# Kernel tuning notes

Measured on AMD Instinct MI355X. Metric: run time of the kernel, lower is better.

The kernel has to match this reference:

```python
import jax, jax.numpy as jnp
import numpy as np

B, S, D, H, O = 8192, 64, 128, 128, 128  # sets, max set size, input_dim, hidden_dim, out_dim


def setup_inputs() -> dict:
    key = jax.random.key(0)
    ks = jax.random.split(key, 10)
    neigh = jax.random.normal(ks[0], (B, S, D), dtype=jnp.float32)
    lengths = jax.random.randint(ks[1], (B,), 1, S + 1)  # each set has >= 1 neighbor

    def lin_w(k, fan_in, fan_out):
        return jax.random.normal(k, (fan_in, fan_out), dtype=jnp.float32) / np.sqrt(fan_in)

    Wq = lin_w(ks[2], D, H); bq = jax.random.normal(ks[3], (H,), dtype=jnp.float32) * 0.01
    Wk = lin_w(ks[4], D, H); bk = jax.random.normal(ks[5], (H,), dtype=jnp.float32) * 0.01
    Wv = lin_w(ks[6], D, H); bv = jax.random.normal(ks[7], (H,), dtype=jnp.float32) * 0.01
    Wo = lin_w(ks[8], H, O); bo = jax.random.normal(ks[9], (O,), dtype=jnp.float32) * 0.01
    return dict(neigh=neigh, lengths=lengths, Wq=Wq, bq=bq, Wk=Wk, bk=bk,
                Wv=Wv, bv=bv, Wo=Wo, bo=bo)


def reference(neigh, lengths, Wq, bq, Wk, bk, Wv, bv, Wo, bo):
    # neigh: [B, S, D] padded ragged sets; lengths: [B] valid neighbor counts.
    q = neigh @ Wq + bq                                   # [B, S, H]
    k = neigh @ Wk + bk                                   # [B, S, H]
    v = neigh @ Wv + bv                                   # [B, S, H]
    # Original divides by sqrt(input_dim) (not hidden_dim) -- kept faithful.
    scores = jnp.einsum('bsh,bth->bst', q, k) / jnp.sqrt(jnp.asarray(D, q.dtype))
    valid = jnp.arange(S)[None, :] < lengths[:, None]     # [B, S] key/row validity
    scores = jnp.where(valid[:, None, :], scores, jnp.finfo(scores.dtype).min)
    attn = jax.nn.softmax(scores, axis=-1)                # [B, S, S]
    atten_out = jnp.einsum('bst,bth->bsh', attn, v)       # [B, S, H]
    o = atten_out @ Wo + bo                               # [B, S, O]
    # Mean-pool over valid rows of each set (torch.mean over dim 0 per set).
    m = valid[:, :, None].astype(o.dtype)
    pooled = jnp.sum(o * m, axis=1) / lengths[:, None].astype(o.dtype)
    return pooled                                         # [B, O]
```

## Files before the change

kernel.cpp:

```cpp
#include <hip/hip_runtime.h>
#include <hip/hip_bf16.h>
#include <cstdint>


typedef __attribute__((ext_vector_type(8))) short bf16x8;
typedef __attribute__((ext_vector_type(4))) float f32x4;

__device__ __forceinline__ unsigned short f2bf(float f) {
    unsigned int u = __builtin_bit_cast(unsigned int, f);
    u += 0x7fffu + ((u >> 16) & 1u);
    return (unsigned short)(u >> 16);
}
__device__ __forceinline__ float bf2f(unsigned short s) {
    unsigned int u = ((unsigned int)s) << 16;
    return __builtin_bit_cast(float, u);
}
__device__ __forceinline__ unsigned cvt_pk_bf16(float lo, float hi) {
    unsigned r;
    asm("v_cvt_pk_bf16_f32 %0, %1, %2" : "=v"(r) : "v"(lo), "v"(hi));
    return r;
}

__global__ __launch_bounds__(256) void setformer_pre(
    const float* __restrict__ Wq, const float* __restrict__ Wk,
    const float* __restrict__ Wv, const float* __restrict__ Wo,
    const float* __restrict__ bq, const float* __restrict__ bv,
    const float* __restrict__ bo,
    unsigned short* __restrict__ MtBf, float* __restrict__ Nmat,
    float* __restrict__ wsv, float* __restrict__ cvec)
{
    __shared__ float sKd[128], sVd[128];
    const int d = blockIdx.x, tid = threadIdx.x;
    if (tid < 128) { sKd[tid] = Wk[d*128 + tid]; sVd[tid] = Wv[d*128 + tid]; }
    __syncthreads();
    const float invs = 0.088388347648318447f;
    if (tid < 128) {
        const int e = tid;
        float acc = 0.f;
        for (int h = 0; h < 128; ++h) acc = fmaf(Wq[e*128 + h], sKd[h], acc);
        MtBf[d*128 + e] = f2bf(acc * invs);
    } else {
        const int o = tid - 128;
        float acc = 0.f;
        for (int h = 0; h < 128; ++h) acc = fmaf(sVd[h], Wo[h*128 + o], acc);
        Nmat[d*128 + o] = acc;
    }
    if (d == 0 && tid < 128) {
        float a = 0.f, c = 0.f;
        for (int h = 0; h < 128; ++h) {
            a = fmaf(Wk[tid*128 + h], bq[h], a);
            c = fmaf(bv[h], Wo[h*128 + tid], c);
        }
        wsv[tid]  = a * invs;
        cvec[tid] = c + bo[tid];
    }
}

__global__ __launch_bounds__(512, 8) void setformer_main(
    const float* __restrict__ neigh, const int* __restrict__ lengths,
    const unsigned short* __restrict__ MtBf,
    const float* __restrict__ wsv, float* __restrict__ yout)
{
    __shared__ unsigned short sX[64 * 128];
    __shared__ unsigned short sG[64 * 128];
    __shared__ float sWp[4][64];
    __shared__ float sW[64];
    __shared__ float sY4[4][128];

    const int tid  = threadIdx.x;
    const int lane = tid & 63;
    const int wv   = tid >> 6;
    const int l15  = lane & 15;
    const int lg   = lane >> 4;
    const int b    = blockIdx.x;

    const char* bB = (const char*)MtBf + (wv*16 + l15) * 256;
    bf16x8 bfr0 = *(const bf16x8*)(bB +   0 + lg*16);
    bf16x8 bfr1 = *(const bf16x8*)(bB +  64 + lg*16);
    bf16x8 bfr2 = *(const bf16x8*)(bB + 128 + lg*16);
    bf16x8 bfr3 = *(const bf16x8*)(bB + 192 + lg*16);
    const float wadd = wsv[wv*16 + l15];

    const float4* np4 = (const float4*)(neigh + (size_t)b * 8192);
    const float4 f0 = np4[tid];

    int L = lengths[b];
    L = max(1, min(64, L));
    const int ST = (L + 15) >> 4;
    const int rr = tid >> 5, c4 = tid & 31;

    float4 f1 = {0,0,0,0}, f2 = {0,0,0,0}, f3 = {0,0,0,0};
    if (rr + 16 < L) f1 = np4[tid + 512];
    if (rr + 32 < L) f2 = np4[tid + 1024];
    if (rr + 48 < L) f3 = np4[tid + 1536];

    if (tid < 256) ((float*)sWp)[tid] = 0.f;

    {
        uint2 v = {0u, 0u};
        if (rr < L) { v.x = cvt_pk_bf16(f0.x, f0.y); v.y = cvt_pk_bf16(f0.z, f0.w); }
        *(uint2*)((char*)sX + rr*256 + ((c4*8) ^ ((rr & 7) << 4))) = v;
        if (ST > 1) {
            const int r = rr + 16;
            uint2 w = {0u, 0u};
            if (r < L) { w.x = cvt_pk_bf16(f1.x, f1.y); w.y = cvt_pk_bf16(f1.z, f1.w); }
            *(uint2*)((char*)sX + r*256 + ((c4*8) ^ ((r & 7) << 4))) = w;
        }
        if (ST > 2) {
            const int r = rr + 32;
            uint2 w = {0u, 0u};
            if (r < L) { w.x = cvt_pk_bf16(f2.x, f2.y); w.y = cvt_pk_bf16(f2.z, f2.w); }
            *(uint2*)((char*)sX + r*256 + ((c4*8) ^ ((r & 7) << 4))) = w;
        }
        if (ST > 3) {
            const int r = rr + 48;
            uint2 w = {0u, 0u};
            if (r < L) { w.x = cvt_pk_bf16(f3.x, f3.y); w.y = cvt_pk_bf16(f3.z, f3.w); }
            *(uint2*)((char*)sX + r*256 + ((c4*8) ^ ((r & 7) << 4))) = w;
        }
    }
    __syncthreads();

    for (int st = 0; st < ST; ++st) {
        const char* aB = (const char*)sX + (st*16 + l15) * 256;
        f32x4 acc = {0.f, 0.f, 0.f, 0.f};
        bf16x8 a0 = *(const bf16x8*)(aB + ((  0 + lg*16) ^ ((l15 & 7) << 4)));
        acc = __builtin_amdgcn_mfma_f32_16x16x32_bf16(a0, bfr0, acc, 0, 0, 0);
        bf16x8 a1 = *(const bf16x8*)(aB + (( 64 + lg*16) ^ ((l15 & 7) << 4)));
        acc = __builtin_amdgcn_mfma_f32_16x16x32_bf16(a1, bfr1, acc, 0, 0, 0);
        bf16x8 a2 = *(const bf16x8*)(aB + ((128 + lg*16) ^ ((l15 & 7) << 4)));
        acc = __builtin_amdgcn_mfma_f32_16x16x32_bf16(a2, bfr2, acc, 0, 0, 0);
        bf16x8 a3 = *(const bf16x8*)(aB + ((192 + lg*16) ^ ((l15 & 7) << 4)));
        acc = __builtin_amdgcn_mfma_f32_16x16x32_bf16(a3, bfr3, acc, 0, 0, 0);
        #pragma unroll
        for (int j = 0; j < 4; ++j) {
            const int gr  = st*16 + lg*4 + j;
            const int gcb = ((wv*16 + l15) * 2) ^ ((gr & 7) << 4);
            const float g = acc[j] + wadd;
            *(unsigned short*)((char*)sG + gr*256 + gcb) =
                (unsigned short)cvt_pk_bf16(g, g);
        }
    }
    __syncthreads();

    if (wv < ST) {
        const char* aB = (const char*)sG + (wv*16 + l15) * 256;
        bf16x8 afr[4];
        #pragma unroll
        for (int kk = 0; kk < 4; ++kk)
            afr[kk] = *(const bf16x8*)(aB + ((kk*64 + lg*16) ^ ((l15 & 7) << 4)));

        f32x4 sc[4];
        #pragma unroll
        for (int tt = 0; tt < 4; ++tt) {
            f32x4 acc = {0.f, 0.f, 0.f, 0.f};
            if (tt < ST) {
                const char* bBt = (const char*)sX + (tt*16 + l15) * 256;
                #pragma unroll
                for (int kk = 0; kk < 4; ++kk) {
                    bf16x8 bfr = *(const bf16x8*)(bBt + ((kk*64 + lg*16) ^ ((l15 & 7) << 4)));
                    acc = __builtin_amdgcn_mfma_f32_16x16x32_bf16(afr[kk], bfr, acc, 0, 0, 0);
                }
            }
            sc[tt] = acc;
        }

        float den[4] = {0.f, 0.f, 0.f, 0.f};
        #pragma unroll
        for (int tt = 0; tt < 4; ++tt) {
            if (tt < ST) {
                const bool tv = (tt*16 + l15) < L;
                #pragma unroll
                for (int j = 0; j < 4; ++j) {
                    float p = tv ? __expf(sc[tt][j]) : 0.f;
                    sc[tt][j] = p;
                    den[j] += p;
                }
            }
        }
        #pragma unroll
        for (int j = 0; j < 4; ++j) {
            #pragma unroll
            for (int off = 1; off < 16; off <<= 1)
                den[j] += __shfl_xor(den[j], off);
        }
        const float invL = 1.0f / (float)L;
        float rinv[4];
        #pragma unroll
        for (int j = 0; j < 4; ++j) {
            const int srow = wv*16 + lg*4 + j;
            rinv[j] = (srow < L) ? (invL / den[j]) : 0.f;
        }
        #pragma unroll
        for (int tt = 0; tt < 4; ++tt) {
            if (tt < ST) {
                float cp = sc[tt][0]*rinv[0] + sc[tt][1]*rinv[1]
                         + sc[tt][2]*rinv[2] + sc[tt][3]*rinv[3];
                cp += __shfl_xor(cp, 16);
                cp += __shfl_xor(cp, 32);
                if (lane < 16) sWp[wv][tt*16 + lane] = cp;
            }
        }
    }
    __syncthreads();

    if (tid < 64)
        sW[tid] = sWp[0][tid] + sWp[1][tid] + sWp[2][tid] + sWp[3][tid];
    __syncthreads();

    {
        const int q = tid >> 7, col = tid & 127;
        float acc = 0.f;
        const int t0 = q * 16, t1 = min(t0 + 16, L);
        for (int t = t0; t < t1; ++t) {
            const unsigned short xv = *(const unsigned short*)
                ((const char*)sX + t*256 + ((col*2) ^ ((t & 7) << 4)));
            acc = fmaf(sW[t], bf2f(xv), acc);
        }
        sY4[q][col] = acc;
    }
    __syncthreads();

    if (tid < 128)
        yout[(size_t)b*128 + tid] = sY4[0][tid] + sY4[1][tid]
                                  + sY4[2][tid] + sY4[3][tid];
}

__global__ __launch_bounds__(256) void setformer_out(
    const float* __restrict__ yin, const float* __restrict__ Nmat,
    const float* __restrict__ cvec, float* __restrict__ out)
{
    __shared__ float sy[16 * 128];
    const int tid = threadIdx.x;
    const size_t r0 = (size_t)blockIdx.x * 16;
    const float4* y4 = (const float4*)(yin + r0 * 128);
    float4* sy4 = (float4*)sy;
    sy4[tid]       = y4[tid];
    sy4[tid + 256] = y4[tid + 256];
    __syncthreads();
    const int col = tid & 127;
    const int rg  = (tid >> 7) * 8;
    float acc[8];
    #pragma unroll
    for (int i = 0; i < 8; ++i) acc[i] = 0.f;
    for (int d = 0; d < 128; d += 2) {
        const float n0 = Nmat[(d+0)*128 + col];
        const float n1 = Nmat[(d+1)*128 + col];
        #pragma unroll
        for (int i = 0; i < 8; ++i) {
            const float2 yv = *(const float2*)&sy[(rg + i)*128 + d];
            acc[i] = fmaf(yv.x, n0, acc[i]);
            acc[i] = fmaf(yv.y, n1, acc[i]);
        }
    }
    const float c = cvec[col];
    #pragma unroll
    for (int i = 0; i < 8; ++i)
        out[(r0 + rg + i)*128 + col] = acc[i] + c;
}

extern "C" void kernel_launch(void* const* d_in, const int* in_sizes, int n_in,
                              void* d_out, int out_size, void* d_ws, size_t ws_size,
                              hipStream_t stream)
{
    const float* neigh   = (const float*)d_in[0];
    const int*   lengths = (const int*)  d_in[1];
    const float* Wq = (const float*)d_in[2];
    const float* bq = (const float*)d_in[3];
    const float* Wk = (const float*)d_in[4];
    const float* Wv = (const float*)d_in[6];
    const float* bv = (const float*)d_in[7];
    const float* Wo = (const float*)d_in[8];
    const float* bo = (const float*)d_in[9];

    const int B = in_sizes[1];

    char* ws = (char*)d_ws;
    unsigned short* MtBf = (unsigned short*)(ws);
    float* Nmat = (float*)(ws + 32768);
    float* wsv  = (float*)(ws + 32768 + 65536);
    float* cvec = (float*)(ws + 32768 + 65536 + 512);
    float* ybuf = (float*)(ws + 32768 + 65536 + 1024);

    hipLaunchKernelGGL(setformer_pre, dim3(128), dim3(256), 0, stream,
                       Wq, Wk, Wv, Wo, bq, bv, bo, MtBf, Nmat, wsv, cvec);
    hipLaunchKernelGGL(setformer_main, dim3(B), dim3(512), 0, stream,
                       neigh, lengths, MtBf, wsv, ybuf);
    hipLaunchKernelGGL(setformer_out, dim3(B / 16), dim3(256), 0, stream,
                       ybuf, Nmat, cvec, (float*)d_out);
}
```

Before: 77.54 us.

## Fuse output projection into main kernel with bf16 N matrix

```diff
diff --git a/kernel.cpp b/kernel.cpp
--- a/kernel.cpp
+++ b/kernel.cpp
@@ -5,6 +5,7 @@
 
 typedef __attribute__((ext_vector_type(8))) short bf16x8;
 typedef __attribute__((ext_vector_type(4))) float f32x4;
+typedef __attribute__((ext_vector_type(4))) unsigned short u16x4;
 
 __device__ __forceinline__ unsigned short f2bf(float f) {
     unsigned int u = __builtin_bit_cast(unsigned int, f);
@@ -26,7 +27,7 @@
     const float* __restrict__ Wv, const float* __restrict__ Wo,
     const float* __restrict__ bq, const float* __restrict__ bv,
     const float* __restrict__ bo,
-    unsigned short* __restrict__ MtBf, float* __restrict__ Nmat,
+    unsigned short* __restrict__ MtBf, unsigned short* __restrict__ NbBf,
     float* __restrict__ wsv, float* __restrict__ cvec)
 {
     __shared__ float sKd[128], sVd[128];
@@ -43,7 +44,7 @@
         const int o = tid - 128;
         float acc = 0.f;
         for (int h = 0; h < 128; ++h) acc = fmaf(sVd[h], Wo[h*128 + o], acc);
-        Nmat[d*128 + o] = acc;
+        NbBf[d*128 + o] = f2bf(acc);
     }
     if (d == 0 && tid < 128) {
         float a = 0.f, c = 0.f;
@@ -58,14 +59,17 @@
 
 __global__ __launch_bounds__(512, 8) void setformer_main(
     const float* __restrict__ neigh, const int* __restrict__ lengths,
-    const unsigned short* __restrict__ MtBf,
-    const float* __restrict__ wsv, float* __restrict__ yout)
+    const unsigned short* __restrict__ MtBf, const float* __restrict__ wsv,
+    const unsigned short* __restrict__ NbBf, const float* __restrict__ cvec,
+    float* __restrict__ out)
 {
     __shared__ unsigned short sX[64 * 128];
     __shared__ unsigned short sG[64 * 128];
     __shared__ float sWp[4][64];
     __shared__ float sW[64];
     __shared__ float sY4[4][128];
+    __shared__ float sYf[128];
+    __shared__ float sOut[128];
 
     const int tid  = threadIdx.x;
     const int lane = tid & 63;
@@ -80,6 +84,8 @@
     bf16x8 bfr2 = *(const bf16x8*)(bB + 128 + lg*16);
     bf16x8 bfr3 = *(const bf16x8*)(bB + 192 + lg*16);
     const float wadd = wsv[wv*16 + l15];
+    float cval = 0.f;
+    if (tid < 128) cval = cvec[tid];
 
     const float4* np4 = (const float4*)(neigh + (size_t)b * 8192);
     const float4 f0 = np4[tid];
@@ -208,6 +214,16 @@
         sW[tid] = sWp[0][tid] + sWp[1][tid] + sWp[2][tid] + sWp[3][tid];
     __syncthreads();
 
+    const int c0 = (tid & 31) * 4;
+    const int dg = tid >> 5;
+    u16x4 nb[8];
+    {
+        const unsigned short* NbRow = NbBf + (dg*8)*128 + c0;
+        #pragma unroll
+        for (int dd = 0; dd < 8; ++dd)
+            nb[dd] = *(const u16x4*)(NbRow + dd*128);
+    }
+
     {
         const int q = tid >> 7, col = tid & 127;
         float acc = 0.f;
@@ -221,42 +237,37 @@
     }
     __syncthreads();
 
-    if (tid < 128)
-        yout[(size_t)b*128 + tid] = sY4[0][tid] + sY4[1][tid]
-                                  + sY4[2][tid] + sY4[3][tid];
-}
-
-__global__ __launch_bounds__(256) void setformer_out(
-    const float* __restrict__ yin, const float* __restrict__ Nmat,
-    const float* __restrict__ cvec, float* __restrict__ out)
-{
-    __shared__ float sy[16 * 128];
-    const int tid = threadIdx.x;
-    const size_t r0 = (size_t)blockIdx.x * 16;
-    const float4* y4 = (const float4*)(yin + r0 * 128);
-    float4* sy4 = (float4*)sy;
-    sy4[tid]       = y4[tid];
-    sy4[tid + 256] = y4[tid + 256];
-    __syncthreads();
-    const int col = tid & 127;
-    const int rg  = (tid >> 7) * 8;
-    float acc[8];
-    #pragma unroll
-    for (int i = 0; i < 8; ++i) acc[i] = 0.f;
-    for (int d = 0; d < 128; d += 2) {
-        const float n0 = Nmat[(d+0)*128 + col];
-        const float n1 = Nmat[(d+1)*128 + col];
-        #pragma unroll
-        for (int i = 0; i < 8; ++i) {
-            const float2 yv = *(const float2*)&sy[(rg + i)*128 + d];
-            acc[i] = fmaf(yv.x, n0, acc[i]);
-            acc[i] = fmaf(yv.y, n1, acc[i]);
-        }
-    }
-    const float c = cvec[col];
-    #pragma unroll
-    for (int i = 0; i < 8; ++i)
-        out[(r0 + rg + i)*128 + col] = acc[i] + c;
+    if (tid < 128) {
+        sYf[tid]  = sY4[0][tid] + sY4[1][tid] + sY4[2][tid] + sY4[3][tid];
+        sOut[tid] = cval;
+    }
+    __syncthreads();
+
+    {
+        float p0 = 0.f, p1 = 0.f, p2 = 0.f, p3 = 0.f;
+        #pragma unroll
+        for (int dd = 0; dd < 8; ++dd) {
+            const float yd = sYf[dg*8 + dd];
+            p0 = fmaf(yd, bf2f(nb[dd].x), p0);
+            p1 = fmaf(yd, bf2f(nb[dd].y), p1);
+            p2 = fmaf(yd, bf2f(nb[dd].z), p2);
+            p3 = fmaf(yd, bf2f(nb[dd].w), p3);
+        }
+        p0 += __shfl_xor(p0, 32);
+        p1 += __shfl_xor(p1, 32);
+        p2 += __shfl_xor(p2, 32);
+        p3 += __shfl_xor(p3, 32);
+        if (lane < 32) {
+            atomicAdd(&sOut[c0 + 0], p0);
+            atomicAdd(&sOut[c0 + 1], p1);
+            atomicAdd(&sOut[c0 + 2], p2);
+            atomicAdd(&sOut[c0 + 3], p3);
+        }
+    }
+    __syncthreads();
+
+    if (tid < 32)
+        *(float4*)(out + (size_t)b*128 + tid*4) = ((const float4*)sOut)[tid];
 }
 
 extern "C" void kernel_launch(void* const* d_in, const int* in_sizes, int n_in,
@@ -277,15 +288,12 @@
 
     char* ws = (char*)d_ws;
     unsigned short* MtBf = (unsigned short*)(ws);
-    float* Nmat = (float*)(ws + 32768);
-    float* wsv  = (float*)(ws + 32768 + 65536);
-    float* cvec = (float*)(ws + 32768 + 65536 + 512);
-    float* ybuf = (float*)(ws + 32768 + 65536 + 1024);
+    unsigned short* NbBf = (unsigned short*)(ws + 32768);
+    float* wsv  = (float*)(ws + 65536);
+    float* cvec = (float*)(ws + 66048);
 
     hipLaunchKernelGGL(setformer_pre, dim3(128), dim3(256), 0, stream,
-                       Wq, Wk, Wv, Wo, bq, bv, bo, MtBf, Nmat, wsv, cvec);
+                       Wq, Wk, Wv, Wo, bq, bv, bo, MtBf, NbBf, wsv, cvec);
     hipLaunchKernelGGL(setformer_main, dim3(B), dim3(512), 0, stream,
-                       neigh, lengths, MtBf, wsv, ybuf);
-    hipLaunchKernelGGL(setformer_out, dim3(B / 16), dim3(256), 0, stream,
-                       ybuf, Nmat, cvec, (float*)d_out);
-}
+                       neigh, lengths, MtBf, wsv, NbBf, cvec, (float*)d_out);
+}
```

Result: slower. 110.5 us (+42.6%).

## Process two sets per block and prefetch the second set's neighbors during the first

Applied to the files above, without the earlier changes.

```diff
diff --git a/kernel.cpp b/kernel.cpp
--- a/kernel.cpp
+++ b/kernel.cpp
@@ -81,149 +81,193 @@
     bf16x8 bfr3 = *(const bf16x8*)(bB + 192 + lg*16);
     const float wadd = wsv[wv*16 + l15];
 
-    const float4* np4 = (const float4*)(neigh + (size_t)b * 8192);
-    const float4 f0 = np4[tid];
-
-    int L = lengths[b];
-    L = max(1, min(64, L));
-    const int ST = (L + 15) >> 4;
+    const float4* np4a = (const float4*)(neigh + (size_t)(2*b) * 8192);
+    const float4 f0 = np4a[tid];
+
+    int L0 = lengths[2*b];     L0 = max(1, min(64, L0));
+    int L1 = lengths[2*b + 1]; L1 = max(1, min(64, L1));
     const int rr = tid >> 5, c4 = tid & 31;
 
     float4 f1 = {0,0,0,0}, f2 = {0,0,0,0}, f3 = {0,0,0,0};
-    if (rr + 16 < L) f1 = np4[tid + 512];
-    if (rr + 32 < L) f2 = np4[tid + 1024];
-    if (rr + 48 < L) f3 = np4[tid + 1536];
+    if (rr + 16 < L0) f1 = np4a[tid + 512];
+    if (rr + 32 < L0) f2 = np4a[tid + 1024];
+    if (rr + 48 < L0) f3 = np4a[tid + 1536];
 
     if (tid < 256) ((float*)sWp)[tid] = 0.f;
 
     {
+        const int ST0 = (L0 + 15) >> 4;
         uint2 v = {0u, 0u};
-        if (rr < L) { v.x = cvt_pk_bf16(f0.x, f0.y); v.y = cvt_pk_bf16(f0.z, f0.w); }
+        if (rr < L0) { v.x = cvt_pk_bf16(f0.x, f0.y); v.y = cvt_pk_bf16(f0.z, f0.w); }
         *(uint2*)((char*)sX + rr*256 + ((c4*8) ^ ((rr & 7) << 4))) = v;
-        if (ST > 1) {
+        if (ST0 > 1) {
             const int r = rr + 16;
             uint2 w = {0u, 0u};
-            if (r < L) { w.x = cvt_pk_bf16(f1.x, f1.y); w.y = cvt_pk_bf16(f1.z, f1.w); }
+            if (r < L0) { w.x = cvt_pk_bf16(f1.x, f1.y); w.y = cvt_pk_bf16(f1.z, f1.w); }
             *(uint2*)((char*)sX + r*256 + ((c4*8) ^ ((r & 7) << 4))) = w;
         }
-        if (ST > 2) {
+        if (ST0 > 2) {
             const int r = rr + 32;
             uint2 w = {0u, 0u};
-            if (r < L) { w.x = cvt_pk_bf16(f2.x, f2.y); w.y = cvt_pk_bf16(f2.z, f2.w); }
+            if (r < L0) { w.x = cvt_pk_bf16(f2.x, f2.y); w.y = cvt_pk_bf16(f2.z, f2.w); }
             *(uint2*)((char*)sX + r*256 + ((c4*8) ^ ((r & 7) << 4))) = w;
         }
-        if (ST > 3) {
+        if (ST0 > 3) {
             const int r = rr + 48;
             uint2 w = {0u, 0u};
-            if (r < L) { w.x = cvt_pk_bf16(f3.x, f3.y); w.y = cvt_pk_bf16(f3.z, f3.w); }
+            if (r < L0) { w.x = cvt_pk_bf16(f3.x, f3.y); w.y = cvt_pk_bf16(f3.z, f3.w); }
             *(uint2*)((char*)sX + r*256 + ((c4*8) ^ ((r & 7) << 4))) = w;
         }
     }
     __syncthreads();
 
-    for (int st = 0; st < ST; ++st) {
-        const char* aB = (const char*)sX + (st*16 + l15) * 256;
-        f32x4 acc = {0.f, 0.f, 0.f, 0.f};
-        bf16x8 a0 = *(const bf16x8*)(aB + ((  0 + lg*16) ^ ((l15 & 7) << 4)));
-        acc = __builtin_amdgcn_mfma_f32_16x16x32_bf16(a0, bfr0, acc, 0, 0, 0);
-        bf16x8 a1 = *(const bf16x8*)(aB + (( 64 + lg*16) ^ ((l15 & 7) << 4)));
-        acc = __builtin_amdgcn_mfma_f32_16x16x32_bf16(a1, bfr1, acc, 0, 0, 0);
-        bf16x8 a2 = *(const bf16x8*)(aB + ((128 + lg*16) ^ ((l15 & 7) << 4)));
-        acc = __builtin_amdgcn_mfma_f32_16x16x32_bf16(a2, bfr2, acc, 0, 0, 0);
-        bf16x8 a3 = *(const bf16x8*)(aB + ((192 + lg*16) ^ ((l15 & 7) << 4)));
-        acc = __builtin_amdgcn_mfma_f32_16x16x32_bf16(a3, bfr3, acc, 0, 0, 0);
-        #pragma unroll
-        for (int j = 0; j < 4; ++j) {
-            const int gr  = st*16 + lg*4 + j;
-            const int gcb = ((wv*16 + l15) * 2) ^ ((gr & 7) << 4);
-            const float g = acc[j] + wadd;
-            *(unsigned short*)((char*)sG + gr*256 + gcb) =
-                (unsigned short)cvt_pk_bf16(g, g);
-        }
-    }
-    __syncthreads();
-
-    if (wv < ST) {
-        const char* aB = (const char*)sG + (wv*16 + l15) * 256;
-        bf16x8 afr[4];
-        #pragma unroll
-        for (int kk = 0; kk < 4; ++kk)
-            afr[kk] = *(const bf16x8*)(aB + ((kk*64 + lg*16) ^ ((l15 & 7) << 4)));
-
-        f32x4 sc[4];
-        #pragma unroll
-        for (int tt = 0; tt < 4; ++tt) {
+    #pragma unroll
+    for (int k = 0; k < 2; ++k) {
+        const int L  = (k == 0) ? L0 : L1;
+        const int ST = (L + 15) >> 4;
+
+        for (int st = 0; st < ST; ++st) {
+            const char* aB = (const char*)sX + (st*16 + l15) * 256;
             f32x4 acc = {0.f, 0.f, 0.f, 0.f};
-            if (tt < ST) {
-                const char* bBt = (const char*)sX + (tt*16 + l15) * 256;
+            bf16x8 a0 = *(const bf16x8*)(aB + ((  0 + lg*16) ^ ((l15 & 7) << 4)));
+            acc = __builtin_amdgcn_mfma_f32_16x16x32_bf16(a0, bfr0, acc, 0, 0, 0);
+            bf16x8 a1 = *(const bf16x8*)(aB + (( 64 + lg*16) ^ ((l15 & 7) << 4)));
+            acc = __builtin_amdgcn_mfma_f32_16x16x32_bf16(a1, bfr1, acc, 0, 0, 0);
+            bf16x8 a2 = *(const bf16x8*)(aB + ((128 + lg*16) ^ ((l15 & 7) << 4)));
+            acc = __builtin_amdgcn_mfma_f32_16x16x32_bf16(a2, bfr2, acc, 0, 0, 0);
+            bf16x8 a3 = *(const bf16x8*)(aB + ((192 + lg*16) ^ ((l15 & 7) << 4)));
+            acc = __builtin_amdgcn_mfma_f32_16x16x32_bf16(a3, bfr3, acc, 0, 0, 0);
+            #pragma unroll
+            for (int j = 0; j < 4; ++j) {
+                const int gr  = st*16 + lg*4 + j;
+                const int gcb = ((wv*16 + l15) * 2) ^ ((gr & 7) << 4);
+                const float g = acc[j] + wadd;
+                *(unsigned short*)((char*)sG + gr*256 + gcb) =
+                    (unsigned short)cvt_pk_bf16(g, g);
+            }
+        }
+        __syncthreads();
+
+        if (wv < ST) {
+            const char* aB = (const char*)sG + (wv*16 + l15) * 256;
+            bf16x8 afr[4];
+            #pragma unroll
+            for (int kk = 0; kk < 4; ++kk)
+                afr[kk] = *(const bf16x8*)(aB + ((kk*64 + lg*16) ^ ((l15 & 7) << 4)));
+
+            f32x4 sc[4];
+            #pragma unroll
+            for (int tt = 0; tt < 4; ++tt) {
+                f32x4 acc = {0.f, 0.f, 0.f, 0.f};
+                if (tt < ST) {
+                    const char* bBt = (const char*)sX + (tt*16 + l15) * 256;
+                    #pragma unroll
+                    for (int kk = 0; kk < 4; ++kk) {
+                        bf16x8 bfr = *(const bf16x8*)(bBt + ((kk*64 + lg*16) ^ ((l15 & 7) << 4)));
+                        acc = __builtin_amdgcn_mfma_f32_16x16x32_bf16(afr[kk], bfr, acc, 0, 0, 0);
+                    }
+                }
+                sc[tt] = acc;
+            }
+
+            float den[4] = {0.f, 0.f, 0.f, 0.f};
+            #pragma unroll
+            for (int tt = 0; tt < 4; ++tt) {
+                if (tt < ST) {
+                    const bool tv = (tt*16 + l15) < L;
+                    #pragma unroll
+                    for (int j = 0; j < 4; ++j) {
+                        float p = tv ? __expf(sc[tt][j]) : 0.f;
+                        sc[tt][j] = p;
+                        den[j] += p;
+                    }
+                }
+            }
+            #pragma unroll
+            for (int j = 0; j < 4; ++j) {
                 #pragma unroll
-                for (int kk = 0; kk < 4; ++kk) {
-                    bf16x8 bfr = *(const bf16x8*)(bBt + ((kk*64 + lg*16) ^ ((l15 & 7) << 4)));
-                    acc = __builtin_amdgcn_mfma_f32_16x16x32_bf16(afr[kk], bfr, acc, 0, 0, 0);
+                for (int off = 1; off < 16; off <<= 1)
+                    den[j] += __shfl_xor(den[j], off);
+            }
+            const float invL = 1.0f / (float)L;
+            float rinv[4];
+            #pragma unroll
+            for (int j = 0; j < 4; ++j) {
+                const int srow = wv*16 + lg*4 + j;
+                rinv[j] = (srow < L) ? (invL / den[j]) : 0.f;
+            }
+            #pragma unroll
+            for (int tt = 0; tt < 4; ++tt) {
+                if (tt < ST) {
+                    float cp = sc[tt][0]*rinv[0] + sc[tt][1]*rinv[1]
+                             + sc[tt][2]*rinv[2] + sc[tt][3]*rinv[3];
+                    cp += __shfl_xor(cp, 16);
+                    cp += __shfl_xor(cp, 32);
+                    if (lane < 16) sWp[wv][tt*16 + lane] = cp;
                 }
             }
-            sc[tt] = acc;
-        }
-
-        float den[4] = {0.f, 0.f, 0.f, 0.f};
-        #pragma unroll
-        for (int tt = 0; tt < 4; ++tt) {
-            if (tt < ST) {
-                const bool tv = (tt*16 + l15) < L;
-                #pragma unroll
-                for (int j = 0; j < 4; ++j) {
-                    float p = tv ? __expf(sc[tt][j]) : 0.f;
-                    sc[tt][j] = p;
-                    den[j] += p;
-                }
-            }
-        }
-        #pragma unroll
-        for (int j = 0; j < 4; ++j) {
-            #pragma unroll
-            for (int off = 1; off < 16; off <<= 1)
-                den[j] += __shfl_xor(den[j], off);
-        }
-        const float invL = 1.0f / (float)L;
-        float rinv[4];
-        #pragma unroll
-        for (int j = 0; j < 4; ++j) {
-            const int srow = wv*16 + lg*4 + j;
-            rinv[j] = (srow < L) ? (invL / den[j]) : 0.f;
-        }
-        #pragma unroll
-        for (int tt = 0; tt < 4; ++tt) {
-            if (tt < ST) {
-                float cp = sc[tt][0]*rinv[0] + sc[tt][1]*rinv[1]
-                         + sc[tt][2]*rinv[2] + sc[tt][3]*rinv[3];
-                cp += __shfl_xor(cp, 16);
-                cp += __shfl_xor(cp, 32);
-                if (lane < 16) sWp[wv][tt*16 + lane] = cp;
-            }
-        }
-    }
-    __syncthreads();
-
-    if (tid < 64)
-        sW[tid] = sWp[0][tid] + sWp[1][tid] + sWp[2][tid] + sWp[3][tid];
-    __syncthreads();
-
-    {
-        const int q = tid >> 7, col = tid & 127;
-        float acc = 0.f;
-        const int t0 = q * 16, t1 = min(t0 + 16, L);
-        for (int t = t0; t < t1; ++t) {
-            const unsigned short xv = *(const unsigned short*)
-                ((const char*)sX + t*256 + ((col*2) ^ ((t & 7) << 4)));
-            acc = fmaf(sW[t], bf2f(xv), acc);
-        }
-        sY4[q][col] = acc;
-    }
-    __syncthreads();
-
-    if (tid < 128)
-        yout[(size_t)b*128 + tid] = sY4[0][tid] + sY4[1][tid]
-                                  + sY4[2][tid] + sY4[3][tid];
+        }
+        __syncthreads();
+
+        if (tid < 64)
+            sW[tid] = sWp[0][tid] + sWp[1][tid] + sWp[2][tid] + sWp[3][tid];
+
+        float4 g0 = {0,0,0,0}, g1 = {0,0,0,0}, g2 = {0,0,0,0}, g3 = {0,0,0,0};
+        if (k == 0) {
+            __builtin_amdgcn_sched_barrier(0);
+            const float4* np4b = (const float4*)(neigh + (size_t)(2*b + 1) * 8192);
+            if (rr      < L1) g0 = np4b[tid];
+            if (rr + 16 < L1) g1 = np4b[tid + 512];
+            if (rr + 32 < L1) g2 = np4b[tid + 1024];
+            if (rr + 48 < L1) g3 = np4b[tid + 1536];
+            __builtin_amdgcn_sched_barrier(0);
+        }
+        __syncthreads();
+
+        {
+            const int q = tid >> 7, col = tid & 127;
+            float acc = 0.f;
+            const int t0 = q * 16, t1 = min(t0 + 16, L);
+            for (int t = t0; t < t1; ++t) {
+                const unsigned short xv = *(const unsigned short*)
+                    ((const char*)sX + t*256 + ((col*2) ^ ((t & 7) << 4)));
+                acc = fmaf(sW[t], bf2f(xv), acc);
+            }
+            sY4[q][col] = acc;
+        }
+        if (tid < 256) ((float*)sWp)[tid] = 0.f;
+        __syncthreads();
+
+        if (tid < 128)
+            yout[(size_t)(2*b + k)*128 + tid] = (sY4[0][tid] + sY4[1][tid])
+                                             + (sY4[2][tid] + sY4[3][tid]);
+
+        if (k == 0) {
+            const int ST1 = (L1 + 15) >> 4;
+            uint2 v = {0u, 0u};
+            if (rr < L1) { v.x = cvt_pk_bf16(g0.x, g0.y); v.y = cvt_pk_bf16(g0.z, g0.w); }
+            *(uint2*)((char*)sX + rr*256 + ((c4*8) ^ ((rr & 7) << 4))) = v;
+            if (ST1 > 1) {
+                const int r = rr + 16;
+                uint2 w = {0u, 0u};
+                if (r < L1) { w.x = cvt_pk_bf16(g1.x, g1.y); w.y = cvt_pk_bf16(g1.z, g1.w); }
+                *(uint2*)((char*)sX + r*256 + ((c4*8) ^ ((r & 7) << 4))) = w;
+            }
+            if (ST1 > 2) {
+                const int r = rr + 32;
+                uint2 w = {0u, 0u};
+                if (r < L1) { w.x = cvt_pk_bf16(g2.x, g2.y); w.y = cvt_pk_bf16(g2.z, g2.w); }
+                *(uint2*)((char*)sX + r*256 + ((c4*8) ^ ((r & 7) << 4))) = w;
+            }
+            if (ST1 > 3) {
+                const int r = rr + 48;
+                uint2 w = {0u, 0u};
+                if (r < L1) { w.x = cvt_pk_bf16(g3.x, g3.y); w.y = cvt_pk_bf16(g3.z, g3.w); }
+                *(uint2*)((char*)sX + r*256 + ((c4*8) ^ ((r & 7) << 4))) = w;
+            }
+            __syncthreads();
+        }
+    }
 }
 
 __global__ __launch_bounds__(256) void setformer_out(
@@ -278,13 +322,13 @@
     char* ws = (char*)d_ws;
     unsigned short* MtBf = (unsigned short*)(ws);
     float* Nmat = (float*)(ws + 32768);
-    float* wsv  = (float*)(ws + 32768 + 65536);
-    float* cvec = (float*)(ws + 32768 + 65536 + 512);
-    float* ybuf = (float*)(ws + 32768 + 65536 + 1024);
+    float* wsv  = (float*)(ws + 98304);
+    float* cvec = (float*)(ws + 98816);
+    float* ybuf = (float*)(ws + 99328);
 
     hipLaunchKernelGGL(setformer_pre, dim3(128), dim3(256), 0, stream,
                        Wq, Wk, Wv, Wo, bq, bv, bo, MtBf, Nmat, wsv, cvec);
-    hipLaunchKernelGGL(setformer_main, dim3(B), dim3(512), 0, stream,
+    hipLaunchKernelGGL(setformer_main, dim3(B / 2), dim3(512), 0, stream,
                        neigh, lengths, MtBf, wsv, ybuf);
     hipLaunchKernelGGL(setformer_out, dim3(B / 16), dim3(256), 0, stream,
                        ybuf, Nmat, cvec, (float*)d_out);
```

Measured after the change: 102.2 us. 31.8% more time.
